# Kernel optimization log

Hardware: AMD Instinct MI355X
Metric: run time of the kernel (lower is better)

## Reference

```python
import jax, jax.numpy as jnp
import numpy as np
from jax import lax

N_NODES = 20000
N_EDGES = 320000
FEAT = 100
N_RULES = 64
T_RULE = 50
H_RNN = 256
RULE_NUMS = 16
NTN_OUT = 200


def setup_inputs() -> dict:
    key = jax.random.key(0)
    ks = iter(jax.random.split(key, 64))
    nrm = lambda shape, s=0.05: jax.random.normal(next(ks), shape, jnp.float32) * s
    inp = {}
    inp["node_features_0"] = jax.random.normal(next(ks), (N_NODES, FEAT), jnp.float32)
    inp["node_features_1"] = jax.random.normal(next(ks), (N_NODES, FEAT), jnp.float32)
    inp["edge_indices_0"] = jax.random.randint(next(ks), (2, N_EDGES), 0, N_NODES)
    inp["edge_indices_1"] = jax.random.randint(next(ks), (2, N_EDGES), 0, N_NODES)
    inp["edge_features_0"] = jax.random.normal(next(ks), (N_EDGES, FEAT), jnp.float32)
    inp["edge_features_1"] = jax.random.normal(next(ks), (N_EDGES, FEAT), jnp.float32)
    inp["rules"] = jax.random.normal(next(ks), (N_RULES, T_RULE, FEAT), jnp.float32)
    # TripleConv 1: edge lin (3*100 -> 100) and nn = mlp (100->100->100)
    inp["c1_lin_W"] = nrm((FEAT, 3 * FEAT)); inp["c1_lin_b"] = jnp.zeros((FEAT,))
    inp["c1_W1"] = nrm((FEAT, FEAT)); inp["c1_b1"] = jnp.zeros((FEAT,))
    inp["c1_W2"] = nrm((FEAT, FEAT)); inp["c1_b2"] = jnp.zeros((FEAT,))
    # TripleConv 2
    inp["c2_lin_W"] = nrm((FEAT, 3 * FEAT)); inp["c2_lin_b"] = jnp.zeros((FEAT,))
    inp["c2_W1"] = nrm((FEAT, FEAT)); inp["c2_b1"] = jnp.zeros((FEAT,))
    inp["c2_W2"] = nrm((FEAT, FEAT)); inp["c2_b2"] = jnp.zeros((FEAT,))
    # NTN (input_dim=100 to match pooled graph vectors, out_dim=200)
    inp["ntn_W"] = nrm((FEAT, FEAT, NTN_OUT))
    inp["ntn_V"] = nrm((NTN_OUT, 2 * FEAT))
    inp["ntn_B"] = jnp.zeros((NTN_OUT,))
    # RuleEmbedding: 2-layer tanh RNN (100 -> 256 -> 256) + Linear(256,100)
    inp["rnn0_Wih"] = nrm((H_RNN, FEAT)); inp["rnn0_Whh"] = nrm((H_RNN, H_RNN))
    inp["rnn0_bih"] = jnp.zeros((H_RNN,)); inp["rnn0_bhh"] = jnp.zeros((H_RNN,))
    inp["rnn1_Wih"] = nrm((H_RNN, H_RNN)); inp["rnn1_Whh"] = nrm((H_RNN, H_RNN))
    inp["rnn1_bih"] = jnp.zeros((H_RNN,)); inp["rnn1_bhh"] = jnp.zeros((H_RNN,))
    inp["rule_lin_W"] = nrm((FEAT, H_RNN)); inp["rule_lin_b"] = jnp.zeros((FEAT,))
    # RuleRanker 100->128->64->1
    inp["rk_W1"] = nrm((128, FEAT)); inp["rk_b1"] = jnp.zeros((128,))
    inp["rk_W2"] = nrm((64, 128)); inp["rk_b2"] = jnp.zeros((64,))
    inp["rk_W3"] = nrm((1, 64)); inp["rk_b3"] = jnp.zeros((1,))
    # Head: fc1 (200 + rule_nums*100 -> 500) -> fc2 (500->100) -> fc3 (100->1)
    inp["fc1_W"] = nrm((500, NTN_OUT + RULE_NUMS * FEAT)); inp["fc1_b"] = jnp.zeros((500,))
    inp["fc2_W"] = nrm((FEAT, 500)); inp["fc2_b"] = jnp.zeros((FEAT,))
    inp["fc3_W"] = nrm((1, FEAT)); inp["fc3_b"] = jnp.zeros((1,))
    return inp


def _triple_conv(x, src, dst, e, lin_W, lin_b, W1, b1, W2, b2):
    # message: relu(Linear(concat(x_i, edge_attr, x_j))); PyG: i=target, j=source
    m = jax.nn.relu(jnp.concatenate([x[dst], e, x[src]], axis=1) @ lin_W.T + lin_b)
    agg = jax.ops.segment_sum(m, dst, num_segments=x.shape[0])  # aggr='add'
    out = agg + x  # (1 + eps) * x_r with eps = 0
    h = jax.nn.relu(out @ W1.T + b1)
    return h @ W2.T + b2  # nn = Sequential(Linear, ReLU, Linear)


def _conv_pass(x, ei, e, c_lin_W, c_lin_b, c_W1, c_b1, c_W2, c_b2,
               d_lin_W, d_lin_b, d_W1, d_b1, d_W2, d_b2):
    src, dst = ei[0], ei[1]
    x = jax.nn.relu(_triple_conv(x, src, dst, e, c_lin_W, c_lin_b, c_W1, c_b1, c_W2, c_b2))
    x = jax.nn.relu(_triple_conv(x, src, dst, e, d_lin_W, d_lin_b, d_W1, d_b1, d_W2, d_b2))
    return x


def _rnn_layer(x_tbf, Wih, Whh, bih, bhh):
    # x_tbf: [T, B, in]; returns all hidden states [T, B, H] and final [B, H]
    h0 = jnp.zeros((x_tbf.shape[1], Whh.shape[0]), x_tbf.dtype)
    def step(h, xt):
        h = jnp.tanh(xt @ Wih.T + bih + h @ Whh.T + bhh)
        return h, h
    hT, ys = lax.scan(step, h0, x_tbf)
    return ys, hT


def reference(node_features_0, node_features_1, edge_indices_0, edge_indices_1,
              edge_features_0, edge_features_1, rules,
              c1_lin_W, c1_lin_b, c1_W1, c1_b1, c1_W2, c1_b2,
              c2_lin_W, c2_lin_b, c2_W1, c2_b1, c2_W2, c2_b2,
              ntn_W, ntn_V, ntn_B,
              rnn0_Wih, rnn0_Whh, rnn0_bih, rnn0_bhh,
              rnn1_Wih, rnn1_Whh, rnn1_bih, rnn1_bhh,
              rule_lin_W, rule_lin_b,
              rk_W1, rk_b1, rk_W2, rk_b2, rk_W3, rk_b3,
              fc1_W, fc1_b, fc2_W, fc2_b, fc3_W, fc3_b):
    # --- rule embedding (all sequences full length => pack/pad is identity) ---
    x = jnp.transpose(rules, (1, 0, 2))  # [T, B, 100]
    ys, _ = _rnn_layer(x, rnn0_Wih, rnn0_Whh, rnn0_bih, rnn0_bhh)
    _, hT = _rnn_layer(ys, rnn1_Wih, rnn1_Whh, rnn1_bih, rnn1_bhh)
    rules_embedding = hT @ rule_lin_W.T + rule_lin_b  # [B, 100]
    # --- rule ranking + top-k ---
    h = jax.nn.relu(rules_embedding @ rk_W1.T + rk_b1)
    h = jax.nn.relu(h @ rk_W2.T + rk_b2)
    rules_score = jax.nn.sigmoid(h @ rk_W3.T + rk_b3)[:, 0]  # [B]
    _, top_idx = lax.top_k(rules_score, RULE_NUMS)
    top_rules_embedding = rules_embedding[top_idx]  # [rule_nums, 100]
    # --- GNN message passing on both graphs ---
    f1 = _conv_pass(node_features_0, edge_indices_0, edge_features_0,
                    c1_lin_W, c1_lin_b, c1_W1, c1_b1, c1_W2, c1_b2,
                    c2_lin_W, c2_lin_b, c2_W1, c2_b1, c2_W2, c2_b2)
    f2 = _conv_pass(node_features_1, edge_indices_1, edge_features_1,
                    c1_lin_W, c1_lin_b, c1_W1, c1_b1, c1_W2, c1_b2,
                    c2_lin_W, c2_lin_b, c2_W1, c2_b1, c2_W2, c2_b2)
    g1 = jnp.sum(f1, axis=0, keepdims=True)  # global_add_pool, single graph -> [1, 100]
    g2 = jnp.sum(f2, axis=0, keepdims=True)
    # --- NTN(g1, g2) ---
    tp = jnp.einsum('ai,ijk,bj->abk', g1, ntn_W, g2)  # [1,1,200]
    concat = jnp.concatenate([g1[:, None, :] * jnp.ones_like(g2)[None, :, :1],
                              g2[None, :, :] * jnp.ones_like(g1)[:, None, :1]], axis=2)
    lin_term = concat @ ntn_V.T  # [1,1,200]
    ntn_out = jax.nn.relu(tp + lin_term + ntn_B).reshape(-1)  # squeeze -> [200]
    # --- scoring head ---
    feat = jnp.concatenate([ntn_out, top_rules_embedding.reshape(-1)])  # [200 + rule_nums*100]
    z = jax.nn.relu(feat @ fc1_W.T + fc1_b)
    z = jax.nn.relu(z @ fc2_W.T + fc2_b)
    score = jax.nn.sigmoid(z @ fc3_W.T + fc3_b)
    return score.reshape(())
```

## Files before the change

kernel.cpp:

```cpp
#include <hip/hip_runtime.h>

typedef unsigned short u16;
typedef unsigned int u32;

#define N_NODES 20000
#define N_EDGES 320000
#define FEAT 100
#define XPAD 112
#define MPAD 104
#define N_RULES 64
#define T_RULE 50
#define H_RNN 256
#define RULE_NUMS 16
#define NTN_OUT 200
#define SCAN_B 79

typedef __attribute__((ext_vector_type(8))) short short8;
typedef __attribute__((ext_vector_type(4))) float f32x4;

__device__ __forceinline__ u16 f2bu(float f) {
  u32 u = __float_as_uint(f);
  u32 r = (u + 0x7fffu + ((u >> 16) & 1u)) >> 16;
  return (u16)r;
}
__device__ __forceinline__ float bu2f(u16 u) {
  return __uint_as_float(((u32)u) << 16);
}
__device__ __forceinline__ u32 pk2(float a, float b) {
  return (u32)f2bu(a) | ((u32)f2bu(b) << 16);
}

__device__ __forceinline__ void lds_st16(void* base, int byteOff, uint4 v) {
  *(uint4*)((char*)base + byteOff) = v;
}
__device__ __forceinline__ short8 lds_ld16(const void* base, int byteOff) {
  return *(const short8*)((const char*)base + byteOff);
}

#define SWZ(row, kByte) (((((row) << 8) + (kByte))) ^ (((row) & 7) << 4))

__device__ __forceinline__ int hs_off(int row, int chunk) {
  return (row << 9) | (((chunk + row * 5) & 31) << 4);
// ... 64 lines not shown
  }
  if (i < N_NODES) off[g * (N_NODES + 1) + i] = buf[tid] - v;
  if (tid == 255) bsum[g * SCAN_B + b] = buf[255];
}

__global__ __launch_bounds__(128) void k_scan2(int* __restrict__ bsum) {
  __shared__ int s[128];
  const int g = blockIdx.y, tid = threadIdx.x;
  const int v = (tid < SCAN_B) ? bsum[g * SCAN_B + tid] : 0;
  s[tid] = v;
  __syncthreads();
  for (int ofs = 1; ofs < 128; ofs <<= 1) {
    const int t = (tid >= ofs) ? s[tid - ofs] : 0;
    __syncthreads();
    s[tid] += t;
    __syncthreads();
  }
  if (tid < SCAN_B) bsum[g * SCAN_B + tid] = s[tid] - v;
}

__global__ __launch_bounds__(256) void k_scan3(const int* __restrict__ bsum,
                                               int* __restrict__ off,
                                               int* __restrict__ cursor) {
  const int g = blockIdx.y, b = blockIdx.x, tid = threadIdx.x;
  const int i = b * 256 + tid;
  if (i < N_NODES) {
    const int o = off[g * (N_NODES + 1) + i] + bsum[g * SCAN_B + b];
    off[g * (N_NODES + 1) + i] = o;
    cursor[g * N_NODES + i] = o;
  }
  if (i == N_NODES) off[g * (N_NODES + 1) + N_NODES] = N_EDGES;
}

__global__ void k_scatter2(const int* __restrict__ d0, const int* __restrict__ d1,
                           int* __restrict__ cursor, int* __restrict__ rank0,
                           int* __restrict__ rank1) {
  const int e = blockIdx.x * blockDim.x + threadIdx.x;
  const int g = blockIdx.y;
  const int* d = g ? d1 : d0;
  if (e < N_EDGES) {
    const int pos = atomicAdd(&cursor[g * N_NODES + d[e]], 1);
    (g ? rank1 : rank0)[e] = pos;
  }
}

template <int VARIANT>
__global__ __launch_bounds__(256) void k_gemm_u(
    const float* __restrict__ Af, const u16* __restrict__ Ab,
    const float* __restrict__ W, const float* __restrict__ b0,
    const float* __restrict__ b1, float* __restrict__ Uout) {
  __shared__ __align__(16) u16 As[64 * 128];
  __shared__ __align__(16) u16 Bs[128 * 128];
  const int tid = threadIdx.x;
  const int lane = tid & 63;
  const int wv = tid >> 6;
  const int l15 = lane & 15;
  const int lhi = lane >> 4;
  const int mb = blockIdx.x * 64;
  const int nb = blockIdx.y * 128;
  const int rb = (wv >> 1) * 32;
  const int cb = (wv & 1) * 64;
  constexpr int KV = VARIANT ? 256 : 100;
  constexpr int NPH = VARIANT ? 2 : 1;

  f32x4 acc[2][4];
  const f32x4 z4 = {0.f, 0.f, 0.f, 0.f};
#pragma unroll
  for (int i = 0; i < 2; ++i)
#pragma unroll
    for (int j = 0; j < 4; ++j) acc[i][j] = z4;

  for (int kc = 0; kc < NPH; ++kc) {
    __syncthreads();
    {
      const int row = tid >> 2;
// ... 295 lines not shown
    short8 af[4], bfr[4];
#pragma unroll
    for (int i = 0; i < 4; ++i) {
      af[i] = lds_ld16(As, SWZ(rb + i * 16 + l15, kByte));
      bfr[i] = lds_ld16(Bs, SWZ(cb + i * 16 + l15, kByte));
    }
#pragma unroll
    for (int i = 0; i < 4; ++i)
#pragma unroll
      for (int j = 0; j < 4; ++j)
        acc[i][j] = __builtin_amdgcn_mfma_f32_16x16x32_bf16(af[i], bfr[j],
                                                            acc[i][j], 0, 0, 0);
  }
  u16* Out = p ? Q : P;
#pragma unroll
  for (int j = 0; j < 4; ++j) {
    const int col = cb + j * 16 + l15;
    if (col >= XPAD) continue;
    const bool valid = col < FEAT;
    const float bias = (valid && !p) ? linB[col] : 0.f;
#pragma unroll
    for (int i = 0; i < 4; ++i) {
      const int row0 = rb + i * 16 + lhi * 4;
#pragma unroll
      for (int q = 0; q < 4; ++q) {
        const int node = n0 + row0 + q;
        if (node < N_NODES)
          Out[(size_t)node * XPAD + col] = valid ? f2bu(acc[i][j][q] + bias) : (u16)0;
      }
    }
  }
}

__global__ __launch_bounds__(256) void k_msgE(
    const float* __restrict__ ef, const u16* __restrict__ Wb,
    const int* __restrict__ srcI, const int* __restrict__ dstI,
    const int* __restrict__ rank, const u16* __restrict__ Pb,
    const u16* __restrict__ Qb, u16* __restrict__ mOut) {
  __shared__ __align__(16) u16 As[64 * 128];
  __shared__ __align__(16) u16 Bs[128 * 128];
  const int tid = threadIdx.x;
  const int lane = tid & 63;
  const int wv = tid >> 6;
  const int l15 = lane & 15;
  const int lhi = lane >> 4;
  const int e0 = blockIdx.x * 64;

  const int rr = tid >> 2;
  const int t4 = tid & 3;
  const int ge = e0 + rr;
  const int dn = dstI[ge];
  const int sn = srcI[ge];
  const int rk = rank[ge];
  uint4 pv[4], qv[4];
#pragma unroll
  for (int c = 0; c < 4; ++c) {
    const int chunk = t4 * 4 + c;
    uint4 z = {0u, 0u, 0u, 0u};
    pv[c] = z; qv[c] = z;
    if (chunk < 14) {
      pv[c] = *(const uint4*)(Pb + (size_t)dn * XPAD + chunk * 8);
      qv[c] = *(const uint4*)(Qb + (size_t)sn * XPAD + chunk * 8);
    }
  }

  {
    const int row = tid >> 2;
    const int k0 = (tid & 3) * 32;
    const float* ar = ef + (size_t)(e0 + row) * FEAT;
#pragma unroll
    for (int c = 0; c < 4; ++c) {
      const int k = k0 + c * 8;
      uint4 v = {0u, 0u, 0u, 0u};
      if (k + 8 <= FEAT) {
        const float4 fa = *(const float4*)(ar + k);
        const float4 fb = *(const float4*)(ar + k + 4);
        v.x = pk2(fa.x, fa.y); v.y = pk2(fa.z, fa.w);
        v.z = pk2(fb.x, fb.y); v.w = pk2(fb.z, fb.w);
      } else if (k < FEAT) {
        const float4 fa = *(const float4*)(ar + k);
        v.x = pk2(fa.x, fa.y); v.y = pk2(fa.z, fa.w);
      }
      lds_st16(As, SWZ(row, k * 2), v);
    }
  }
  {
    const int row = tid >> 1;
    const int hf = tid & 1;
    const uint4* wr = (const uint4*)(Wb + 16384 + (size_t)row * 128);
#pragma unroll
    for (int q = 0; q < 8; ++q) {
      const int cc = hf * 8 + q;
      lds_st16(Bs, SWZ(row, cc * 16), wr[cc]);
    }
  }
  __syncthreads();

  const int rb = (wv >> 1) * 32;
  const int cb = (wv & 1) * 64;
  f32x4 acc[2][4];
  const f32x4 z4 = {0.f, 0.f, 0.f, 0.f};
#pragma unroll
  for (int i = 0; i < 2; ++i)
#pragma unroll
    for (int j = 0; j < 4; ++j) acc[i][j] = z4;
#pragma unroll
  for (int s = 0; s < 4; ++s) {
    const int kByte = s * 64 + lhi * 16;
    short8 af[2], bfr[4];
#pragma unroll
    for (int i = 0; i < 2; ++i)
      af[i] = lds_ld16(As, SWZ(rb + i * 16 + l15, kByte));
#pragma unroll
    for (int j = 0; j < 4; ++j)
      bfr[j] = lds_ld16(Bs, SWZ(cb + j * 16 + l15, kByte));
#pragma unroll
    for (int i = 0; i < 2; ++i)
#pragma unroll
      for (int j = 0; j < 4; ++j)
        acc[i][j] = __builtin_amdgcn_mfma_f32_16x16x32_bf16(af[i], bfr[j],
                                                            acc[i][j], 0, 0, 0);
  }
  __syncthreads();
#pragma unroll
  for (int i = 0; i < 2; ++i) {
#pragma unroll
    for (int j = 0; j < 4; ++j) {
      const int col = cb + j * 16 + l15;
#pragma unroll
      for (int q = 0; q < 4; ++q) {
        const int row = rb + i * 16 + lhi * 4 + q;
        *(u16*)((char*)As + (SWZ(row, col * 2))) = f2bu(acc[i][j][q]);
      }
    }
  }
  __syncthreads();
#pragma unroll
  for (int c = 0; c < 4; ++c) {
    const int chunk = t4 * 4 + c;
    if (chunk > 12) break;
    const short8 ev = lds_ld16(As, SWZ(rr, chunk * 16));
    const uint4 e4 = *(const uint4*)&ev;
    const uint4 p4 = pv[c];
    const uint4 q4 = qv[c];
    uint4 o;
    {
      float v0 = bu2f((u16)(e4.x & 0xffffu)) + bu2f((u16)(p4.x & 0xffffu)) +
                 bu2f((u16)(q4.x & 0xffffu));
      float v1 = bu2f((u16)(e4.x >> 16)) + bu2f((u16)(p4.x >> 16)) +
                 bu2f((u16)(q4.x >> 16));
      o.x = pk2(v0 > 0.f ? v0 : 0.f, v1 > 0.f ? v1 : 0.f);
      float v2 = bu2f((u16)(e4.y & 0xffffu)) + bu2f((u16)(p4.y & 0xffffu)) +
                 bu2f((u16)(q4.y & 0xffffu));
      float v3 = bu2f((u16)(e4.y >> 16)) + bu2f((u16)(p4.y >> 16)) +
                 bu2f((u16)(q4.y >> 16));
      o.y = pk2(v2 > 0.f ? v2 : 0.f, v3 > 0.f ? v3 : 0.f);
      float v4 = bu2f((u16)(e4.z & 0xffffu)) + bu2f((u16)(p4.z & 0xffffu)) +
                 bu2f((u16)(q4.z & 0xffffu));
      float v5 = bu2f((u16)(e4.z >> 16)) + bu2f((u16)(p4.z >> 16)) +
                 bu2f((u16)(q4.z >> 16));
      o.z = pk2(v4 > 0.f ? v4 : 0.f, v5 > 0.f ? v5 : 0.f);
      float v6 = bu2f((u16)(e4.w & 0xffffu)) + bu2f((u16)(p4.w & 0xffffu)) +
                 bu2f((u16)(q4.w & 0xffffu));
      float v7 = bu2f((u16)(e4.w >> 16)) + bu2f((u16)(p4.w >> 16)) +
                 bu2f((u16)(q4.w >> 16));
      o.w = pk2(v6 > 0.f ? v6 : 0.f, v7 > 0.f ? v7 : 0.f);
    }
    *(uint4*)(mOut + (size_t)rk * MPAD + chunk * 8) = o;
  }
}

__global__ __launch_bounds__(256) void k_agg(
    const u16* __restrict__ mPerm, const int* __restrict__ off,
    const u16* __restrict__ xb, u16* __restrict__ aggb) {
  const int tid = threadIdx.x;
  const int ln = tid >> 5;
  const int j = tid & 31;
  const int n = blockIdx.x * 8 + ln;
  if (j >= 28) return;
  u16* outp = aggb + (size_t)n * XPAD + j * 4;
  if (j >= 26) {
    uint2 z = {0u, 0u};
    *(uint2*)outp = z;
    return;
  }
  const int p0 = off[n], p1 = off[n + 1];
  float a0 = 0.f, a1 = 0.f, a2 = 0.f, a3 = 0.f;
  const u16* mp = mPerm + (size_t)j * 4;
  int p = p0;
  for (; p + 3 < p1; p += 4) {
    const uint2 u0 = *(const uint2*)(mp + (size_t)p * MPAD);
    const uint2 u1 = *(const uint2*)(mp + (size_t)(p + 1) * MPAD);
    const uint2 u2 = *(const uint2*)(mp + (size_t)(p + 2) * MPAD);
    const uint2 u3 = *(const uint2*)(mp + (size_t)(p + 3) * MPAD);
    a0 += bu2f((u16)(u0.x & 0xffffu)) + bu2f((u16)(u1.x & 0xffffu)) +
          bu2f((u16)(u2.x & 0xffffu)) + bu2f((u16)(u3.x & 0xffffu));
    a1 += bu2f((u16)(u0.x >> 16)) + bu2f((u16)(u1.x >> 16)) +
          bu2f((u16)(u2.x >> 16)) + bu2f((u16)(u3.x >> 16));
    a2 += bu2f((u16)(u0.y & 0xffffu)) + bu2f((u16)(u1.y & 0xffffu)) +
          bu2f((u16)(u2.y & 0xffffu)) + bu2f((u16)(u3.y & 0xffffu));
    a3 += bu2f((u16)(u0.y >> 16)) + bu2f((u16)(u1.y >> 16)) +
          bu2f((u16)(u2.y >> 16)) + bu2f((u16)(u3.y >> 16));
  }
  for (; p < p1; ++p) {
    const uint2 u0 = *(const uint2*)(mp + (size_t)p * MPAD);
    a0 += bu2f((u16)(u0.x & 0xffffu));
    a1 += bu2f((u16)(u0.x >> 16));
    a2 += bu2f((u16)(u0.y & 0xffffu));
    a3 += bu2f((u16)(u0.y >> 16));
  }
  const uint2 xv = *(const uint2*)(xb + (size_t)n * XPAD + j * 4);
  a0 += bu2f((u16)(xv.x & 0xffffu));
  a1 += bu2f((u16)(xv.x >> 16));
  a2 += bu2f((u16)(xv.y & 0xffffu));
  a3 += bu2f((u16)(xv.y >> 16));
  uint2 o;
  o.x = pk2(a0, a1);
  o.y = pk2(a2, a3);
  *(uint2*)outp = o;
}

__global__ __launch_bounds__(256) void k_mlp(
    const u16* __restrict__ aggb, const u16* __restrict__ W1b,
    const float* __restrict__ b1, const u16* __restrict__ W2b,
    const float* __restrict__ b2, u16* __restrict__ xbout) {
  __shared__ __align__(16) u16 As[128 * 128];
  __shared__ __align__(16) u16 Bs[128 * 128];
  const int tid = threadIdx.x;
  const int lane = tid & 63;
  const int wv = tid >> 6;
  const int l15 = lane & 15;
  const int lhi = lane >> 4;
  const int n0 = blockIdx.x * 128;
  const int rStage = tid >> 1;
  const int hf = tid & 1;
  const int rb = (wv >> 1) * 64;
  const int cb = (wv & 1) * 64;
  const f32x4 z4 = {0.f, 0.f, 0.f, 0.f};

  {
    const int node = n0 + rStage;
    const bool ok = node < N_NODES;
    const uint4* xr = (const uint4*)(aggb + (size_t)node * XPAD);
#pragma unroll
    for (int q = 0; q < 8; ++q) {
      const int cc = hf * 8 + q;
      uint4 v = {0u, 0u, 0u, 0u};
      if (ok && cc < 14) v = xr[cc];
      lds_st16(As, SWZ(rStage, cc * 16), v);
    }
  }
  {
    const uint4* wr = (const uint4*)(W1b + (size_t)rStage * 128);
#pragma unroll
    for (int q = 0; q < 8; ++q) {
      const int cc = hf * 8 + q;
      lds_st16(Bs, SWZ(rStage, cc * 16), wr[cc]);
    }
  }
  __syncthreads();

  f32x4 acc[4][4];
#pragma unroll
  for (int i = 0; i < 4; ++i)
#pragma unroll
    for (int j = 0; j < 4; ++j) acc[i][j] = z4;
#pragma unroll
  for (int s = 0; s < 4; ++s) {
    const int kByte = s * 64 + lhi * 16;
    short8 af[4], bfr[4];
#pragma unroll
    for (int i = 0; i < 4; ++i) {
      af[i] = lds_ld16(As, SWZ(rb + i * 16 + l15, kByte));
      bfr[i] = lds_ld16(Bs, SWZ(cb + i * 16 + l15, kByte));
    }
#pragma unroll
    for (int i = 0; i < 4; ++i)
#pragma unroll
      for (int j = 0; j < 4; ++j)
        acc[i][j] = __builtin_amdgcn_mfma_f32_16x16x32_bf16(af[i], bfr[j],
                                                            acc[i][j], 0, 0, 0);
// ... 178 lines not shown
  for (int l = 0; l < 2; ++l)
    for (int k = 0; k < 6; ++k) cw[l][k] = (const float*)d_in[7 + l * 6 + k];
  const float* ntnW = (const float*)d_in[19];
  const float* ntnV = (const float*)d_in[20];
  const float* ntnB = (const float*)d_in[21];
  const float* r0Wih = (const float*)d_in[22];
  const float* r0Whh = (const float*)d_in[23];
  const float* r0bih = (const float*)d_in[24];
  const float* r0bhh = (const float*)d_in[25];
  const float* r1Wih = (const float*)d_in[26];
  const float* r1Whh = (const float*)d_in[27];
  const float* r1bih = (const float*)d_in[28];
  const float* r1bhh = (const float*)d_in[29];
  const float* rlW = (const float*)d_in[30];
  const float* rlb = (const float*)d_in[31];
  const float* rkW1 = (const float*)d_in[32];
  const float* rkb1 = (const float*)d_in[33];
  const float* rkW2 = (const float*)d_in[34];
  const float* rkb2 = (const float*)d_in[35];
  const float* rkW3 = (const float*)d_in[36];
  const float* rkb3 = (const float*)d_in[37];
  const float* fc1W = (const float*)d_in[38];
  const float* fc1b = (const float*)d_in[39];
  const float* fc2W = (const float*)d_in[40];
  const float* fc2b = (const float*)d_in[41];
  const float* fc3W = (const float*)d_in[42];
  const float* fc3b = (const float*)d_in[43];

  char* base = (char*)d_ws;
  size_t woff = 0;
#define WS_ALLOC(T, NAME, BYTES) \
  T* NAME = (T*)(base + woff);   \
  woff = (woff + (size_t)(BYTES) + 255) & ~(size_t)255;
  WS_ALLOC(u16, m_buf, (size_t)N_EDGES * MPAD * 2)
  WS_ALLOC(u16, xb0, (size_t)N_NODES * XPAD * 2)
  WS_ALLOC(u16, xb1, (size_t)N_NODES * XPAD * 2)
  WS_ALLOC(u16, Pbuf, (size_t)N_NODES * XPAD * 2)
  WS_ALLOC(u16, Qbuf, (size_t)N_NODES * XPAD * 2)
  WS_ALLOC(u16, aggb, (size_t)N_NODES * XPAD * 2)
  WS_ALLOC(u16, Wb0, (size_t)3 * 128 * 128 * 2)
  WS_ALLOC(u16, Wb1, (size_t)3 * 128 * 128 * 2)
  WS_ALLOC(u16, Wm, (size_t)4 * 128 * 128 * 2)
  WS_ALLOC(int, offAll, (size_t)2 * (N_NODES + 1) * 4)
  WS_ALLOC(int, cursor, (size_t)2 * N_NODES * 4)
  WS_ALLOC(int, bsum, (size_t)2 * SCAN_B * 4)
  WS_ALLOC(int, rank0, (size_t)N_EDGES * 4)
  WS_ALLOC(int, rank1, (size_t)N_EDGES * 4)
  WS_ALLOC(float, emb, (size_t)N_RULES * FEAT * 4)
  WS_ALLOC(float, scores, (size_t)N_RULES * 4)
  WS_ALLOC(int, topidx, (size_t)RULE_NUMS * 4)
  WS_ALLOC(float, gtp, (size_t)(2 * FEAT + NTN_OUT) * 4)
#undef WS_ALLOC
  u16* xb[2] = {xb0, xb1};
  int* rankg[2] = {rank0, rank1};
  u16* Wbl[2] = {Wb0, Wb1};
  float* gv = gtp;
  float* tp = gtp + 200;

  float* U   = (float*)m_buf;
  u16*   ys  = (u16*)((char*)m_buf + 3276800);
  float* hT  = (float*)((char*)m_buf + 4915200);
  float* featWS = (float*)((char*)m_buf + 4980736);
  float* z1WS   = (float*)((char*)m_buf + 4988160);

  hipMemsetAsync(cursor, 0, (size_t)2 * N_NODES * 4, stream);
  hipMemsetAsync(gtp, 0, (size_t)(2 * FEAT + NTN_OUT) * 4, stream);

  k_prep<<<2048, 256, 0, stream>>>(nf[0], nf[1], xb[0], xb[1]);
  k_wprep<<<192, 256, 0, stream>>>(cw[0][0], Wb0);
  k_wprep<<<192, 256, 0, stream>>>(cw[1][0], Wb1);
  k_wprep_sq<<<64, 256, 0, stream>>>(cw[0][2], Wm);
  k_wprep_sq<<<64, 256, 0, stream>>>(cw[0][4], Wm + 16384);
  k_wprep_sq<<<64, 256, 0, stream>>>(cw[1][2], Wm + 2 * 16384);
  k_wprep_sq<<<64, 256, 0, stream>>>(cw[1][4], Wm + 3 * 16384);

  const int* src0 = ei[0];
  const int* src1 = ei[1];
  const int* dst0 = ei[0] + N_EDGES;
  const int* dst1 = ei[1] + N_EDGES;
  k_count2<<<dim3(1250, 2), 256, 0, stream>>>(dst0, dst1, cursor);
  k_scan1<<<dim3(SCAN_B, 2), 256, 0, stream>>>(cursor, offAll, bsum);
  k_scan2<<<dim3(1, 2), 128, 0, stream>>>(bsum);
  k_scan3<<<dim3(SCAN_B, 2), 256, 0, stream>>>(bsum, offAll, cursor);
  k_scatter2<<<dim3(1250, 2), 256, 0, stream>>>(dst0, dst1, cursor, rank0, rank1);

  {
    dim3 gg(50, 2);
    k_gemm_u<0><<<gg, 256, 0, stream>>>(rules, nullptr, r0Wih, r0bih, r0bhh, U);
    k_rec<1><<<4, 512, 0, stream>>>(U, r0Whh, ys, nullptr);
    k_gemm_u<1><<<gg, 256, 0, stream>>>(nullptr, ys, r1Wih, r1bih, r1bhh, U);
    k_rec<0><<<4, 512, 0, stream>>>(U, r1Whh, nullptr, hT);
    k_rulelin<<<N_RULES, 128, 0, stream>>>(hT, rlW, rlb, emb);
  }
  k_ranker<<<N_RULES, 128, 0, stream>>>(emb, rkW1, rkb1, rkW2, rkb2, rkW3, rkb3,
                                        scores);
  k_topk<<<1, 64, 0, stream>>>(scores, topidx);

  for (int g = 0; g < 2; ++g) {
    const int* srcp = ei[g];
    const int* dstp = ei[g] + N_EDGES;
    const int* offg = offAll + g * (N_NODES + 1);
    for (int l = 0; l < 2; ++l) {
      k_nodegemm<<<dim3(157, 2), 256, 0, stream>>>(xb[g], Wbl[l], cw[l][1],
                                                   Pbuf, Qbuf);
      k_msgE<<<5000, 256, 0, stream>>>(ef[g], Wbl[l], srcp, dstp, rankg[g],
                                       Pbuf, Qbuf, m_buf);
      k_agg<<<2500, 256, 0, stream>>>(m_buf, offg, xb[g], aggb);
      k_mlp<<<157, 256, 0, stream>>>(aggb, Wm + (size_t)(2 * l) * 16384, cw[l][3],
                                     Wm + (size_t)(2 * l + 1) * 16384, cw[l][5],
                                     xb[g]);
    }
    k_pool<<<200, 128, 0, stream>>>(xb[g], gv + g * FEAT);
  }

  k_ntn<<<FEAT, 256, 0, stream>>>(ntnW, gv, gv + FEAT, tp);
  k_feat<<<1, 256, 0, stream>>>(tp, gv, ntnV, ntnB, emb, topidx, featWS);
  k_fc1<<<125, 256, 0, stream>>>(featWS, fc1W, fc1b, z1WS);
  k_head2<<<1, 128, 0, stream>>>(z1WS, fc2W, fc2b, fc3W, fc3b, (float*)d_out);
}
```

Measured before the change: 877.6 us.

## Fuse edge message GEMM with destination-sorted segmented atomic aggregation

The edge scatter now writes dst-sorted edge, source and destination lists. The message kernel processes edges in that sorted order and reduces consecutive same-destination rows in shared memory. It then adds them into an fp32 node buffer with atomics, so the per-edge message buffer and the separate aggregation kernel are gone. Edge weights are loaded straight into registers instead of shared memory, and the self-feature add moves into the MLP's staging step. In exchange it adds a memset per layer, atomic traffic, and gathered (non-coalesced) edge-feature reads.

```diff
diff --git a/kernel.cpp b/kernel.cpp
--- a/kernel.cpp
+++ b/kernel.cpp
@@ -7,7 +7,7 @@
 #define N_EDGES 320000
 #define FEAT 100
 #define XPAD 112
-#define MPAD 104
+#define AGGP 112
 #define N_RULES 64
 #define T_RULE 50
 #define H_RNN 256
@@ -138,15 +138,22 @@
   if (i == N_NODES) off[g * (N_NODES + 1) + N_NODES] = N_EDGES;
 }
 
-__global__ void k_scatter2(const int* __restrict__ d0, const int* __restrict__ d1,
-                           int* __restrict__ cursor, int* __restrict__ rank0,
-                           int* __restrict__ rank1) {
+__global__ void k_scatter2(const int* __restrict__ s0, const int* __restrict__ d0,
+                           const int* __restrict__ s1, const int* __restrict__ d1,
+                           int* __restrict__ cursor,
+                           int* __restrict__ el0, int* __restrict__ el1,
+                           int* __restrict__ sp0, int* __restrict__ sp1,
+                           int* __restrict__ dp0, int* __restrict__ dp1) {
   const int e = blockIdx.x * blockDim.x + threadIdx.x;
   const int g = blockIdx.y;
   const int* d = g ? d1 : d0;
+  const int* s = g ? s1 : s0;
   if (e < N_EDGES) {
-    const int pos = atomicAdd(&cursor[g * N_NODES + d[e]], 1);
-    (g ? rank1 : rank0)[e] = pos;
+    const int dn = d[e];
+    const int pos = atomicAdd(&cursor[g * N_NODES + dn], 1);
+    (g ? el1 : el0)[pos] = e;
+    (g ? sp1 : sp0)[pos] = s[e];
+    (g ? dp1 : dp0)[pos] = dn;
   }
 }
 
@@ -508,26 +515,25 @@
   }
 }
 
-__global__ __launch_bounds__(256) void k_msgE(
+__global__ __launch_bounds__(256, 2) void k_msgagg(
     const float* __restrict__ ef, const u16* __restrict__ Wb,
-    const int* __restrict__ srcI, const int* __restrict__ dstI,
-    const int* __restrict__ rank, const u16* __restrict__ Pb,
-    const u16* __restrict__ Qb, u16* __restrict__ mOut) {
+    const int* __restrict__ elist, const int* __restrict__ spos,
+    const int* __restrict__ dpos, const u16* __restrict__ Pb,
+    const u16* __restrict__ Qb, float* __restrict__ aggf) {
   __shared__ __align__(16) u16 As[64 * 128];
-  __shared__ __align__(16) u16 Bs[128 * 128];
+  __shared__ int dpS[64];
   const int tid = threadIdx.x;
   const int lane = tid & 63;
   const int wv = tid >> 6;
   const int l15 = lane & 15;
   const int lhi = lane >> 4;
-  const int e0 = blockIdx.x * 64;
+  const int p0 = blockIdx.x * 64;
 
   const int rr = tid >> 2;
   const int t4 = tid & 3;
-  const int ge = e0 + rr;
-  const int dn = dstI[ge];
-  const int sn = srcI[ge];
-  const int rk = rank[ge];
+  const int dn = dpos[p0 + rr];
+  const int sn = spos[p0 + rr];
+  if (tid < 64) dpS[tid] = dpos[p0 + tid];
   uint4 pv[4], qv[4];
 #pragma unroll
   for (int c = 0; c < 4; ++c) {
@@ -539,11 +545,24 @@
       qv[c] = *(const uint4*)(Qb + (size_t)sn * XPAD + chunk * 8);
     }
   }
-
+  const int rb = (wv >> 1) * 32;
+  const int cb = (wv & 1) * 64;
+  short8 bf[4][4];
+  {
+    const u16* wbase = Wb + 16384;
+#pragma unroll
+    for (int jt = 0; jt < 4; ++jt) {
+      const u16* wr = wbase + (size_t)(cb + jt * 16 + l15) * 128;
+#pragma unroll
+      for (int s = 0; s < 4; ++s)
+        bf[jt][s] = *(const short8*)(wr + s * 32 + lhi * 8);
+    }
+  }
   {
     const int row = tid >> 2;
     const int k0 = (tid & 3) * 32;
-    const float* ar = ef + (size_t)(e0 + row) * FEAT;
+    const int e = elist[p0 + row];
+    const float* ar = ef + (size_t)e * FEAT;
 #pragma unroll
     for (int c = 0; c < 4; ++c) {
       const int k = k0 + c * 8;
@@ -560,20 +579,8 @@
       lds_st16(As, SWZ(row, k * 2), v);
     }
   }
-  {
-    const int row = tid >> 1;
-    const int hf = tid & 1;
-    const uint4* wr = (const uint4*)(Wb + 16384 + (size_t)row * 128);
-#pragma unroll
-    for (int q = 0; q < 8; ++q) {
-      const int cc = hf * 8 + q;
-      lds_st16(Bs, SWZ(row, cc * 16), wr[cc]);
-    }
-  }
-  __syncthreads();
-
-  const int rb = (wv >> 1) * 32;
-  const int cb = (wv & 1) * 64;
+  __syncthreads();
+
   f32x4 acc[2][4];
   const f32x4 z4 = {0.f, 0.f, 0.f, 0.f};
 #pragma unroll
@@ -583,18 +590,15 @@
 #pragma unroll
   for (int s = 0; s < 4; ++s) {
     const int kByte = s * 64 + lhi * 16;
-    short8 af[2], bfr[4];
+    short8 af[2];
 #pragma unroll
     for (int i = 0; i < 2; ++i)
       af[i] = lds_ld16(As, SWZ(rb + i * 16 + l15, kByte));
 #pragma unroll
-    for (int j = 0; j < 4; ++j)
-      bfr[j] = lds_ld16(Bs, SWZ(cb + j * 16 + l15, kByte));
-#pragma unroll
     for (int i = 0; i < 2; ++i)
 #pragma unroll
       for (int j = 0; j < 4; ++j)
-        acc[i][j] = __builtin_amdgcn_mfma_f32_16x16x32_bf16(af[i], bfr[j],
+        acc[i][j] = __builtin_amdgcn_mfma_f32_16x16x32_bf16(af[i], bf[j][s],
                                                             acc[i][j], 0, 0, 0);
   }
   __syncthreads();
@@ -620,86 +624,63 @@
     const uint4 p4 = pv[c];
     const uint4 q4 = qv[c];
     uint4 o;
-    {
-      float v0 = bu2f((u16)(e4.x & 0xffffu)) + bu2f((u16)(p4.x & 0xffffu)) +
-                 bu2f((u16)(q4.x & 0xffffu));
-      float v1 = bu2f((u16)(e4.x >> 16)) + bu2f((u16)(p4.x >> 16)) +
-                 bu2f((u16)(q4.x >> 16));
-      o.x = pk2(v0 > 0.f ? v0 : 0.f, v1 > 0.f ? v1 : 0.f);
-      float v2 = bu2f((u16)(e4.y & 0xffffu)) + bu2f((u16)(p4.y & 0xffffu)) +
-                 bu2f((u16)(q4.y & 0xffffu));
-      float v3 = bu2f((u16)(e4.y >> 16)) + bu2f((u16)(p4.y >> 16)) +
-                 bu2f((u16)(q4.y >> 16));
-      o.y = pk2(v2 > 0.f ? v2 : 0.f, v3 > 0.f ? v3 : 0.f);
-      float v4 = bu2f((u16)(e4.z & 0xffffu)) + bu2f((u16)(p4.z & 0xffffu)) +
-                 bu2f((u16)(q4.z & 0xffffu));
-      float v5 = bu2f((u16)(e4.z >> 16)) + bu2f((u16)(p4.z >> 16)) +
-                 bu2f((u16)(q4.z >> 16));
-      o.z = pk2(v4 > 0.f ? v4 : 0.f, v5 > 0.f ? v5 : 0.f);
-      float v6 = bu2f((u16)(e4.w & 0xffffu)) + bu2f((u16)(p4.w & 0xffffu)) +
-                 bu2f((u16)(q4.w & 0xffffu));
-      float v7 = bu2f((u16)(e4.w >> 16)) + bu2f((u16)(p4.w >> 16)) +
-                 bu2f((u16)(q4.w >> 16));
-      o.w = pk2(v6 > 0.f ? v6 : 0.f, v7 > 0.f ? v7 : 0.f);
-    }
-    *(uint4*)(mOut + (size_t)rk * MPAD + chunk * 8) = o;
-  }
-}
-
-__global__ __launch_bounds__(256) void k_agg(
-    const u16* __restrict__ mPerm, const int* __restrict__ off,
-    const u16* __restrict__ xb, u16* __restrict__ aggb) {
-  const int tid = threadIdx.x;
-  const int ln = tid >> 5;
-  const int j = tid & 31;
-  const int n = blockIdx.x * 8 + ln;
-  if (j >= 28) return;
-  u16* outp = aggb + (size_t)n * XPAD + j * 4;
-  if (j >= 26) {
-    uint2 z = {0u, 0u};
-    *(uint2*)outp = z;
-    return;
-  }
-  const int p0 = off[n], p1 = off[n + 1];
-  float a0 = 0.f, a1 = 0.f, a2 = 0.f, a3 = 0.f;
-  const u16* mp = mPerm + (size_t)j * 4;
-  int p = p0;
-  for (; p + 3 < p1; p += 4) {
-    const uint2 u0 = *(const uint2*)(mp + (size_t)p * MPAD);
-    const uint2 u1 = *(const uint2*)(mp + (size_t)(p + 1) * MPAD);
-    const uint2 u2 = *(const uint2*)(mp + (size_t)(p + 2) * MPAD);
-    const uint2 u3 = *(const uint2*)(mp + (size_t)(p + 3) * MPAD);
-    a0 += bu2f((u16)(u0.x & 0xffffu)) + bu2f((u16)(u1.x & 0xffffu)) +
-          bu2f((u16)(u2.x & 0xffffu)) + bu2f((u16)(u3.x & 0xffffu));
-    a1 += bu2f((u16)(u0.x >> 16)) + bu2f((u16)(u1.x >> 16)) +
-          bu2f((u16)(u2.x >> 16)) + bu2f((u16)(u3.x >> 16));
-    a2 += bu2f((u16)(u0.y & 0xffffu)) + bu2f((u16)(u1.y & 0xffffu)) +
-          bu2f((u16)(u2.y & 0xffffu)) + bu2f((u16)(u3.y & 0xffffu));
-    a3 += bu2f((u16)(u0.y >> 16)) + bu2f((u16)(u1.y >> 16)) +
-          bu2f((u16)(u2.y >> 16)) + bu2f((u16)(u3.y >> 16));
-  }
-  for (; p < p1; ++p) {
-    const uint2 u0 = *(const uint2*)(mp + (size_t)p * MPAD);
-    a0 += bu2f((u16)(u0.x & 0xffffu));
-    a1 += bu2f((u16)(u0.x >> 16));
-    a2 += bu2f((u16)(u0.y & 0xffffu));
-    a3 += bu2f((u16)(u0.y >> 16));
-  }
-  const uint2 xv = *(const uint2*)(xb + (size_t)n * XPAD + j * 4);
-  a0 += bu2f((u16)(xv.x & 0xffffu));
-  a1 += bu2f((u16)(xv.x >> 16));
-  a2 += bu2f((u16)(xv.y & 0xffffu));
-  a3 += bu2f((u16)(xv.y >> 16));
-  uint2 o;
-  o.x = pk2(a0, a1);
-  o.y = pk2(a2, a3);
-  *(uint2*)outp = o;
+    float v0 = bu2f((u16)(e4.x & 0xffffu)) + bu2f((u16)(p4.x & 0xffffu)) +
+               bu2f((u16)(q4.x & 0xffffu));
+    float v1 = bu2f((u16)(e4.x >> 16)) + bu2f((u16)(p4.x >> 16)) +
+               bu2f((u16)(q4.x >> 16));
+    o.x = pk2(v0 > 0.f ? v0 : 0.f, v1 > 0.f ? v1 : 0.f);
+    float v2 = bu2f((u16)(e4.y & 0xffffu)) + bu2f((u16)(p4.y & 0xffffu)) +
+               bu2f((u16)(q4.y & 0xffffu));
+    float v3 = bu2f((u16)(e4.y >> 16)) + bu2f((u16)(p4.y >> 16)) +
+               bu2f((u16)(q4.y >> 16));
+    o.y = pk2(v2 > 0.f ? v2 : 0.f, v3 > 0.f ? v3 : 0.f);
+    float v4 = bu2f((u16)(e4.z & 0xffffu)) + bu2f((u16)(p4.z & 0xffffu)) +
+               bu2f((u16)(q4.z & 0xffffu));
+    float v5 = bu2f((u16)(e4.z >> 16)) + bu2f((u16)(p4.z >> 16)) +
+               bu2f((u16)(q4.z >> 16));
+    o.z = pk2(v4 > 0.f ? v4 : 0.f, v5 > 0.f ? v5 : 0.f);
+    float v6 = bu2f((u16)(e4.w & 0xffffu)) + bu2f((u16)(p4.w & 0xffffu)) +
+               bu2f((u16)(q4.w & 0xffffu));
+    float v7 = bu2f((u16)(e4.w >> 16)) + bu2f((u16)(p4.w >> 16)) +
+               bu2f((u16)(q4.w >> 16));
+    o.w = pk2(v6 > 0.f ? v6 : 0.f, v7 > 0.f ? v7 : 0.f);
+    lds_st16(As, SWZ(rr, chunk * 16), o);
+  }
+  __syncthreads();
+  if (tid < 104) {
+    const int c = tid % 13;
+    const int g = tid / 13;
+    const int r0 = g * 8;
+    float a[8] = {0.f, 0.f, 0.f, 0.f, 0.f, 0.f, 0.f, 0.f};
+    int curNode = dpS[r0];
+    for (int r = r0; r < r0 + 8; ++r) {
+      const int nd = dpS[r];
+      if (nd != curNode) {
+        float* ap = aggf + (size_t)curNode * AGGP + c * 8;
+#pragma unroll
+        for (int i = 0; i < 8; ++i) atomicAdd(ap + i, a[i]);
+#pragma unroll
+        for (int i = 0; i < 8; ++i) a[i] = 0.f;
+        curNode = nd;
+      }
+      const short8 mv = lds_ld16(As, SWZ(r, c * 16));
+      const uint4 m4 = *(const uint4*)&mv;
+      a[0] += bu2f((u16)(m4.x & 0xffffu)); a[1] += bu2f((u16)(m4.x >> 16));
+      a[2] += bu2f((u16)(m4.y & 0xffffu)); a[3] += bu2f((u16)(m4.y >> 16));
+      a[4] += bu2f((u16)(m4.z & 0xffffu)); a[5] += bu2f((u16)(m4.z >> 16));
+      a[6] += bu2f((u16)(m4.w & 0xffffu)); a[7] += bu2f((u16)(m4.w >> 16));
+    }
+    float* ap = aggf + (size_t)curNode * AGGP + c * 8;
+#pragma unroll
+    for (int i = 0; i < 8; ++i) atomicAdd(ap + i, a[i]);
+  }
 }
 
 __global__ __launch_bounds__(256) void k_mlp(
-    const u16* __restrict__ aggb, const u16* __restrict__ W1b,
-    const float* __restrict__ b1, const u16* __restrict__ W2b,
-    const float* __restrict__ b2, u16* __restrict__ xbout) {
+    const float* __restrict__ aggf, const u16* __restrict__ xb,
+    const u16* __restrict__ W1b, const float* __restrict__ b1,
+    const u16* __restrict__ W2b, const float* __restrict__ b2,
+    u16* __restrict__ xbout) {
   __shared__ __align__(16) u16 As[128 * 128];
   __shared__ __align__(16) u16 Bs[128 * 128];
   const int tid = threadIdx.x;
@@ -717,12 +698,25 @@
   {
     const int node = n0 + rStage;
     const bool ok = node < N_NODES;
-    const uint4* xr = (const uint4*)(aggb + (size_t)node * XPAD);
+    const float* ar = aggf + (size_t)node * AGGP;
+    const u16* xr = xb + (size_t)node * XPAD;
 #pragma unroll
     for (int q = 0; q < 8; ++q) {
       const int cc = hf * 8 + q;
       uint4 v = {0u, 0u, 0u, 0u};
-      if (ok && cc < 14) v = xr[cc];
+      if (ok && cc < 14) {
+        const float4 fa = *(const float4*)(ar + cc * 8);
+        const float4 fb = *(const float4*)(ar + cc * 8 + 4);
+        const uint4 xv = *(const uint4*)(xr + cc * 8);
+        v.x = pk2(fa.x + bu2f((u16)(xv.x & 0xffffu)),
+                  fa.y + bu2f((u16)(xv.x >> 16)));
+        v.y = pk2(fa.z + bu2f((u16)(xv.y & 0xffffu)),
+                  fa.w + bu2f((u16)(xv.y >> 16)));
+        v.z = pk2(fb.x + bu2f((u16)(xv.z & 0xffffu)),
+                  fb.y + bu2f((u16)(xv.z >> 16)));
+        v.w = pk2(fb.z + bu2f((u16)(xv.w & 0xffffu)),
+                  fb.w + bu2f((u16)(xv.w >> 16)));
+      }
       lds_st16(As, SWZ(rStage, cc * 16), v);
     }
   }
@@ -967,36 +961,42 @@
 #define WS_ALLOC(T, NAME, BYTES) \
   T* NAME = (T*)(base + woff);   \
   woff = (woff + (size_t)(BYTES) + 255) & ~(size_t)255;
-  WS_ALLOC(u16, m_buf, (size_t)N_EDGES * MPAD * 2)
+  WS_ALLOC(char, rnn_buf, (size_t)5242880)
   WS_ALLOC(u16, xb0, (size_t)N_NODES * XPAD * 2)
   WS_ALLOC(u16, xb1, (size_t)N_NODES * XPAD * 2)
   WS_ALLOC(u16, Pbuf, (size_t)N_NODES * XPAD * 2)
   WS_ALLOC(u16, Qbuf, (size_t)N_NODES * XPAD * 2)
-  WS_ALLOC(u16, aggb, (size_t)N_NODES * XPAD * 2)
+  WS_ALLOC(float, aggf, (size_t)N_NODES * AGGP * 4)
   WS_ALLOC(u16, Wb0, (size_t)3 * 128 * 128 * 2)
   WS_ALLOC(u16, Wb1, (size_t)3 * 128 * 128 * 2)
   WS_ALLOC(u16, Wm, (size_t)4 * 128 * 128 * 2)
   WS_ALLOC(int, offAll, (size_t)2 * (N_NODES + 1) * 4)
   WS_ALLOC(int, cursor, (size_t)2 * N_NODES * 4)
   WS_ALLOC(int, bsum, (size_t)2 * SCAN_B * 4)
-  WS_ALLOC(int, rank0, (size_t)N_EDGES * 4)
-  WS_ALLOC(int, rank1, (size_t)N_EDGES * 4)
+  WS_ALLOC(int, el0, (size_t)N_EDGES * 4)
+  WS_ALLOC(int, el1, (size_t)N_EDGES * 4)
+  WS_ALLOC(int, sp0, (size_t)N_EDGES * 4)
+  WS_ALLOC(int, sp1, (size_t)N_EDGES * 4)
+  WS_ALLOC(int, dp0, (size_t)N_EDGES * 4)
+  WS_ALLOC(int, dp1, (size_t)N_EDGES * 4)
   WS_ALLOC(float, emb, (size_t)N_RULES * FEAT * 4)
   WS_ALLOC(float, scores, (size_t)N_RULES * 4)
   WS_ALLOC(int, topidx, (size_t)RULE_NUMS * 4)
   WS_ALLOC(float, gtp, (size_t)(2 * FEAT + NTN_OUT) * 4)
 #undef WS_ALLOC
   u16* xb[2] = {xb0, xb1};
-  int* rankg[2] = {rank0, rank1};
+  int* elg[2] = {el0, el1};
+  int* spg[2] = {sp0, sp1};
+  int* dpg[2] = {dp0, dp1};
   u16* Wbl[2] = {Wb0, Wb1};
   float* gv = gtp;
   float* tp = gtp + 200;
 
-  float* U   = (float*)m_buf;
-  u16*   ys  = (u16*)((char*)m_buf + 3276800);
-  float* hT  = (float*)((char*)m_buf + 4915200);
-  float* featWS = (float*)((char*)m_buf + 4980736);
-  float* z1WS   = (float*)((char*)m_buf + 4988160);
+  float* U   = (float*)rnn_buf;
+  u16*   ys  = (u16*)(rnn_buf + 3276800);
+  float* hT  = (float*)(rnn_buf + 4915200);
+  float* featWS = (float*)(rnn_buf + 4980736);
+  float* z1WS   = (float*)(rnn_buf + 4988160);
 
   hipMemsetAsync(cursor, 0, (size_t)2 * N_NODES * 4, stream);
   hipMemsetAsync(gtp, 0, (size_t)(2 * FEAT + NTN_OUT) * 4, stream);
@@ -1017,7 +1017,8 @@
   k_scan1<<<dim3(SCAN_B, 2), 256, 0, stream>>>(cursor, offAll, bsum);
   k_scan2<<<dim3(1, 2), 128, 0, stream>>>(bsum);
   k_scan3<<<dim3(SCAN_B, 2), 256, 0, stream>>>(bsum, offAll, cursor);
-  k_scatter2<<<dim3(1250, 2), 256, 0, stream>>>(dst0, dst1, cursor, rank0, rank1);
+  k_scatter2<<<dim3(1250, 2), 256, 0, stream>>>(src0, dst0, src1, dst1, cursor,
+                                                el0, el1, sp0, sp1, dp0, dp1);
 
   {
     dim3 gg(50, 2);
@@ -1032,18 +1033,15 @@
   k_topk<<<1, 64, 0, stream>>>(scores, topidx);
 
   for (int g = 0; g < 2; ++g) {
-    const int* srcp = ei[g];
-    const int* dstp = ei[g] + N_EDGES;
-    const int* offg = offAll + g * (N_NODES + 1);
     for (int l = 0; l < 2; ++l) {
+      hipMemsetAsync(aggf, 0, (size_t)N_NODES * AGGP * 4, stream);
       k_nodegemm<<<dim3(157, 2), 256, 0, stream>>>(xb[g], Wbl[l], cw[l][1],
                                                    Pbuf, Qbuf);
-      k_msgE<<<5000, 256, 0, stream>>>(ef[g], Wbl[l], srcp, dstp, rankg[g],
-                                       Pbuf, Qbuf, m_buf);
-      k_agg<<<2500, 256, 0, stream>>>(m_buf, offg, xb[g], aggb);
-      k_mlp<<<157, 256, 0, stream>>>(aggb, Wm + (size_t)(2 * l) * 16384, cw[l][3],
-                                     Wm + (size_t)(2 * l + 1) * 16384, cw[l][5],
-                                     xb[g]);
+      k_msgagg<<<5000, 256, 0, stream>>>(ef[g], Wbl[l], elg[g], spg[g], dpg[g],
+                                         Pbuf, Qbuf, aggf);
+      k_mlp<<<157, 256, 0, stream>>>(aggf, xb[g], Wm + (size_t)(2 * l) * 16384,
+                                     cw[l][3], Wm + (size_t)(2 * l + 1) * 16384,
+                                     cw[l][5], xb[g]);
     }
     k_pool<<<200, 128, 0, stream>>>(xb[g], gv + g * FEAT);
   }
```

New measurement: 1.495 ms. 70.3% more time.

## Process edges in destination-sorted order and keep edge weight fragments in registers

Applied to the files above, without the earlier changes.

The scatter pass now writes, for each destination-sorted slot, the original edge id plus its source and destination node. The message kernel iterates over sorted positions, so its output writes become contiguous and gathers of the destination node features get locality. The cost is an indirect read of the edge features. The weight tile is no longer staged in shared memory: each wave loads its bf16 B fragments straight into registers, which cuts LDS use to raise occupancy (launch bounds 256,4). The change also trims the P/Q gather to 13 chunks and adds extra index arrays to the workspace.

```diff
diff --git a/kernel.cpp b/kernel.cpp
--- a/kernel.cpp
+++ b/kernel.cpp
@@ -138,15 +138,22 @@
   if (i == N_NODES) off[g * (N_NODES + 1) + N_NODES] = N_EDGES;
 }
 
-__global__ void k_scatter2(const int* __restrict__ d0, const int* __restrict__ d1,
-                           int* __restrict__ cursor, int* __restrict__ rank0,
-                           int* __restrict__ rank1) {
+__global__ void k_scatter2(const int* __restrict__ s0, const int* __restrict__ d0,
+                           const int* __restrict__ s1, const int* __restrict__ d1,
+                           int* __restrict__ cursor,
+                           int* __restrict__ el0, int* __restrict__ el1,
+                           int* __restrict__ sp0, int* __restrict__ sp1,
+                           int* __restrict__ dp0, int* __restrict__ dp1) {
   const int e = blockIdx.x * blockDim.x + threadIdx.x;
   const int g = blockIdx.y;
   const int* d = g ? d1 : d0;
+  const int* s = g ? s1 : s0;
   if (e < N_EDGES) {
-    const int pos = atomicAdd(&cursor[g * N_NODES + d[e]], 1);
-    (g ? rank1 : rank0)[e] = pos;
+    const int dn = d[e];
+    const int pos = atomicAdd(&cursor[g * N_NODES + dn], 1);
+    (g ? el1 : el0)[pos] = e;
+    (g ? sp1 : sp0)[pos] = s[e];
+    (g ? dp1 : dp0)[pos] = dn;
   }
 }
 
@@ -508,42 +515,51 @@
   }
 }
 
-__global__ __launch_bounds__(256) void k_msgE(
+__global__ __launch_bounds__(256, 4) void k_msgE2(
     const float* __restrict__ ef, const u16* __restrict__ Wb,
-    const int* __restrict__ srcI, const int* __restrict__ dstI,
-    const int* __restrict__ rank, const u16* __restrict__ Pb,
+    const int* __restrict__ elist, const int* __restrict__ spos,
+    const int* __restrict__ dpos, const u16* __restrict__ Pb,
     const u16* __restrict__ Qb, u16* __restrict__ mOut) {
   __shared__ __align__(16) u16 As[64 * 128];
-  __shared__ __align__(16) u16 Bs[128 * 128];
   const int tid = threadIdx.x;
   const int lane = tid & 63;
   const int wv = tid >> 6;
   const int l15 = lane & 15;
   const int lhi = lane >> 4;
-  const int e0 = blockIdx.x * 64;
-
+  const int p0 = blockIdx.x * 64;
   const int rr = tid >> 2;
   const int t4 = tid & 3;
-  const int ge = e0 + rr;
-  const int dn = dstI[ge];
-  const int sn = srcI[ge];
-  const int rk = rank[ge];
+
+  const int dn = dpos[p0 + rr];
+  const int sn = spos[p0 + rr];
   uint4 pv[4], qv[4];
 #pragma unroll
   for (int c = 0; c < 4; ++c) {
     const int chunk = t4 * 4 + c;
     uint4 z = {0u, 0u, 0u, 0u};
     pv[c] = z; qv[c] = z;
-    if (chunk < 14) {
+    if (chunk < 13) {
       pv[c] = *(const uint4*)(Pb + (size_t)dn * XPAD + chunk * 8);
       qv[c] = *(const uint4*)(Qb + (size_t)sn * XPAD + chunk * 8);
     }
   }
-
+  const int rb = (wv >> 1) * 32;
+  const int cb = (wv & 1) * 64;
+  short8 bf[4][4];
   {
-    const int row = tid >> 2;
-    const int k0 = (tid & 3) * 32;
-    const float* ar = ef + (size_t)(e0 + row) * FEAT;
+    const u16* wbase = Wb + 16384;
+#pragma unroll
+    for (int jt = 0; jt < 4; ++jt) {
+      const u16* wr = wbase + (size_t)(cb + jt * 16 + l15) * 128;
+#pragma unroll
+      for (int s = 0; s < 4; ++s)
+        bf[jt][s] = *(const short8*)(wr + s * 32 + lhi * 8);
+    }
+  }
+  {
+    const int e = elist[p0 + rr];
+    const int k0 = t4 * 32;
+    const float* ar = ef + (size_t)e * FEAT;
 #pragma unroll
     for (int c = 0; c < 4; ++c) {
       const int k = k0 + c * 8;
@@ -557,23 +573,11 @@
         const float4 fa = *(const float4*)(ar + k);
         v.x = pk2(fa.x, fa.y); v.y = pk2(fa.z, fa.w);
       }
-      lds_st16(As, SWZ(row, k * 2), v);
-    }
-  }
-  {
-    const int row = tid >> 1;
-    const int hf = tid & 1;
-    const uint4* wr = (const uint4*)(Wb + 16384 + (size_t)row * 128);
-#pragma unroll
-    for (int q = 0; q < 8; ++q) {
-      const int cc = hf * 8 + q;
-      lds_st16(Bs, SWZ(row, cc * 16), wr[cc]);
-    }
-  }
-  __syncthreads();
-
-  const int rb = (wv >> 1) * 32;
-  const int cb = (wv & 1) * 64;
+      lds_st16(As, SWZ(rr, k * 2), v);
+    }
+  }
+  __syncthreads();
+
   f32x4 acc[2][4];
   const f32x4 z4 = {0.f, 0.f, 0.f, 0.f};
 #pragma unroll
@@ -583,18 +587,15 @@
 #pragma unroll
   for (int s = 0; s < 4; ++s) {
     const int kByte = s * 64 + lhi * 16;
-    short8 af[2], bfr[4];
+    short8 af[2];
 #pragma unroll
     for (int i = 0; i < 2; ++i)
       af[i] = lds_ld16(As, SWZ(rb + i * 16 + l15, kByte));
 #pragma unroll
-    for (int j = 0; j < 4; ++j)
-      bfr[j] = lds_ld16(Bs, SWZ(cb + j * 16 + l15, kByte));
-#pragma unroll
     for (int i = 0; i < 2; ++i)
 #pragma unroll
       for (int j = 0; j < 4; ++j)
-        acc[i][j] = __builtin_amdgcn_mfma_f32_16x16x32_bf16(af[i], bfr[j],
+        acc[i][j] = __builtin_amdgcn_mfma_f32_16x16x32_bf16(af[i], bf[j][s],
                                                             acc[i][j], 0, 0, 0);
   }
   __syncthreads();
@@ -620,29 +621,27 @@
     const uint4 p4 = pv[c];
     const uint4 q4 = qv[c];
     uint4 o;
-    {
-      float v0 = bu2f((u16)(e4.x & 0xffffu)) + bu2f((u16)(p4.x & 0xffffu)) +
-                 bu2f((u16)(q4.x & 0xffffu));
-      float v1 = bu2f((u16)(e4.x >> 16)) + bu2f((u16)(p4.x >> 16)) +
-                 bu2f((u16)(q4.x >> 16));
-      o.x = pk2(v0 > 0.f ? v0 : 0.f, v1 > 0.f ? v1 : 0.f);
-      float v2 = bu2f((u16)(e4.y & 0xffffu)) + bu2f((u16)(p4.y & 0xffffu)) +
-                 bu2f((u16)(q4.y & 0xffffu));
-      float v3 = bu2f((u16)(e4.y >> 16)) + bu2f((u16)(p4.y >> 16)) +
-                 bu2f((u16)(q4.y >> 16));
-      o.y = pk2(v2 > 0.f ? v2 : 0.f, v3 > 0.f ? v3 : 0.f);
-      float v4 = bu2f((u16)(e4.z & 0xffffu)) + bu2f((u16)(p4.z & 0xffffu)) +
-                 bu2f((u16)(q4.z & 0xffffu));
-      float v5 = bu2f((u16)(e4.z >> 16)) + bu2f((u16)(p4.z >> 16)) +
-                 bu2f((u16)(q4.z >> 16));
-      o.z = pk2(v4 > 0.f ? v4 : 0.f, v5 > 0.f ? v5 : 0.f);
-      float v6 = bu2f((u16)(e4.w & 0xffffu)) + bu2f((u16)(p4.w & 0xffffu)) +
-                 bu2f((u16)(q4.w & 0xffffu));
-      float v7 = bu2f((u16)(e4.w >> 16)) + bu2f((u16)(p4.w >> 16)) +
-                 bu2f((u16)(q4.w >> 16));
-      o.w = pk2(v6 > 0.f ? v6 : 0.f, v7 > 0.f ? v7 : 0.f);
-    }
-    *(uint4*)(mOut + (size_t)rk * MPAD + chunk * 8) = o;
+    float v0 = bu2f((u16)(e4.x & 0xffffu)) + bu2f((u16)(p4.x & 0xffffu)) +
+               bu2f((u16)(q4.x & 0xffffu));
+    float v1 = bu2f((u16)(e4.x >> 16)) + bu2f((u16)(p4.x >> 16)) +
+               bu2f((u16)(q4.x >> 16));
+    o.x = pk2(v0 > 0.f ? v0 : 0.f, v1 > 0.f ? v1 : 0.f);
+    float v2 = bu2f((u16)(e4.y & 0xffffu)) + bu2f((u16)(p4.y & 0xffffu)) +
+               bu2f((u16)(q4.y & 0xffffu));
+    float v3 = bu2f((u16)(e4.y >> 16)) + bu2f((u16)(p4.y >> 16)) +
+               bu2f((u16)(q4.y >> 16));
+    o.y = pk2(v2 > 0.f ? v2 : 0.f, v3 > 0.f ? v3 : 0.f);
+    float v4 = bu2f((u16)(e4.z & 0xffffu)) + bu2f((u16)(p4.z & 0xffffu)) +
+               bu2f((u16)(q4.z & 0xffffu));
+    float v5 = bu2f((u16)(e4.z >> 16)) + bu2f((u16)(p4.z >> 16)) +
+               bu2f((u16)(q4.z >> 16));
+    o.z = pk2(v4 > 0.f ? v4 : 0.f, v5 > 0.f ? v5 : 0.f);
+    float v6 = bu2f((u16)(e4.w & 0xffffu)) + bu2f((u16)(p4.w & 0xffffu)) +
+               bu2f((u16)(q4.w & 0xffffu));
+    float v7 = bu2f((u16)(e4.w >> 16)) + bu2f((u16)(p4.w >> 16)) +
+               bu2f((u16)(q4.w >> 16));
+    o.w = pk2(v6 > 0.f ? v6 : 0.f, v7 > 0.f ? v7 : 0.f);
+    *(uint4*)(mOut + (size_t)(p0 + rr) * MPAD + chunk * 8) = o;
   }
 }
 
@@ -979,15 +978,21 @@
   WS_ALLOC(int, offAll, (size_t)2 * (N_NODES + 1) * 4)
   WS_ALLOC(int, cursor, (size_t)2 * N_NODES * 4)
   WS_ALLOC(int, bsum, (size_t)2 * SCAN_B * 4)
-  WS_ALLOC(int, rank0, (size_t)N_EDGES * 4)
-  WS_ALLOC(int, rank1, (size_t)N_EDGES * 4)
+  WS_ALLOC(int, el0, (size_t)N_EDGES * 4)
+  WS_ALLOC(int, el1, (size_t)N_EDGES * 4)
+  WS_ALLOC(int, sp0, (size_t)N_EDGES * 4)
+  WS_ALLOC(int, sp1, (size_t)N_EDGES * 4)
+  WS_ALLOC(int, dp0, (size_t)N_EDGES * 4)
+  WS_ALLOC(int, dp1, (size_t)N_EDGES * 4)
   WS_ALLOC(float, emb, (size_t)N_RULES * FEAT * 4)
   WS_ALLOC(float, scores, (size_t)N_RULES * 4)
   WS_ALLOC(int, topidx, (size_t)RULE_NUMS * 4)
   WS_ALLOC(float, gtp, (size_t)(2 * FEAT + NTN_OUT) * 4)
 #undef WS_ALLOC
   u16* xb[2] = {xb0, xb1};
-  int* rankg[2] = {rank0, rank1};
+  int* elg[2] = {el0, el1};
+  int* spg[2] = {sp0, sp1};
+  int* dpg[2] = {dp0, dp1};
   u16* Wbl[2] = {Wb0, Wb1};
   float* gv = gtp;
   float* tp = gtp + 200;
@@ -1017,7 +1022,8 @@
   k_scan1<<<dim3(SCAN_B, 2), 256, 0, stream>>>(cursor, offAll, bsum);
   k_scan2<<<dim3(1, 2), 128, 0, stream>>>(bsum);
   k_scan3<<<dim3(SCAN_B, 2), 256, 0, stream>>>(bsum, offAll, cursor);
-  k_scatter2<<<dim3(1250, 2), 256, 0, stream>>>(dst0, dst1, cursor, rank0, rank1);
+  k_scatter2<<<dim3(1250, 2), 256, 0, stream>>>(src0, dst0, src1, dst1, cursor,
+                                                el0, el1, sp0, sp1, dp0, dp1);
 
   {
     dim3 gg(50, 2);
@@ -1032,14 +1038,12 @@
   k_topk<<<1, 64, 0, stream>>>(scores, topidx);
 
   for (int g = 0; g < 2; ++g) {
-    const int* srcp = ei[g];
-    const int* dstp = ei[g] + N_EDGES;
     const int* offg = offAll + g * (N_NODES + 1);
     for (int l = 0; l < 2; ++l) {
       k_nodegemm<<<dim3(157, 2), 256, 0, stream>>>(xb[g], Wbl[l], cw[l][1],
                                                    Pbuf, Qbuf);
-      k_msgE<<<5000, 256, 0, stream>>>(ef[g], Wbl[l], srcp, dstp, rankg[g],
-                                       Pbuf, Qbuf, m_buf);
+      k_msgE2<<<5000, 256, 0, stream>>>(ef[g], Wbl[l], elg[g], spg[g], dpg[g],
+                                        Pbuf, Qbuf, m_buf);
       k_agg<<<2500, 256, 0, stream>>>(m_buf, offg, xb[g], aggb);
       k_mlp<<<157, 256, 0, stream>>>(aggb, Wm + (size_t)(2 * l) * 16384, cw[l][3],
                                      Wm + (size_t)(2 * l + 1) * 16384, cw[l][5],
```

New measurement: 948.1 us. +8.0%, slower.
